# Kernel optimization log

Hardware: AMD Instinct MI355X
Metric: run time of the kernel (lower is better)

## Reference

```python
import jax, jax.numpy as jnp
import numpy as np

EMBED = 768
HEADS = 12
D_K = EMBED // HEADS  # 64


def setup_inputs() -> dict:
    key = jax.random.key(0)
    ks = jax.random.split(key, 9)
    w_scale = EMBED ** -0.5
    inp = {
        "x": jax.random.normal(ks[0], (128, 256, 1, EMBED), dtype=jnp.float32),
        "Wq": jax.random.normal(ks[1], (EMBED, EMBED), dtype=jnp.float32) * w_scale,
        "bq": jax.random.normal(ks[2], (EMBED,), dtype=jnp.float32) * 0.02,
        "Wk": jax.random.normal(ks[3], (EMBED, EMBED), dtype=jnp.float32) * w_scale,
        "bk": jax.random.normal(ks[4], (EMBED,), dtype=jnp.float32) * 0.02,
        "Wv": jax.random.normal(ks[5], (EMBED, EMBED), dtype=jnp.float32) * w_scale,
        "bv": jax.random.normal(ks[6], (EMBED,), dtype=jnp.float32) * 0.02,
        "Wo": jax.random.normal(ks[7], (EMBED, EMBED), dtype=jnp.float32) * w_scale,
        "bo": jax.random.normal(ks[8], (EMBED,), dtype=jnp.float32) * 0.02,
    }
    return inp


def reference(x, Wq, bq, Wk, bk, Wv, bv, Wo, bo):
    # x: (n_rows r, n_cols i/j, batch n, embed)
    R, C, B, E = x.shape
    H, Dk = HEADS, D_K
    # tied-row scaling: d_k^{-1/2} / sqrt(n_rows)
    scaling = (Dk ** -0.5) / np.sqrt(R).astype(np.float32)

    q = (x @ Wq.T + bq).reshape(R, C, B, H, Dk) * scaling
    k = (x @ Wk.T + bk).reshape(R, C, B, H, Dk)
    v = (x @ Wv.T + bv).reshape(R, C, B, H, Dk)

    # scores summed over rows r and head dim d -> (h, n, i, j)
    scores = jnp.einsum('rinhd,rjnhd->hnij', q, k)
    probs = jax.nn.softmax(scores, axis=-1)  # dropout p=0 -> identity

    # shared attention applied per row
    c = jnp.einsum('hnij,rjnhd->rinhd', probs, v).reshape(R, C, B, E)
    out = c @ Wo.T + bo
    return (out, probs)
```

## Files before the change

### kernel.cpp

```cpp
#include <hip/hip_runtime.h>
#include <math.h>

typedef short bf16x8 __attribute__((ext_vector_type(8)));
typedef float f32x4 __attribute__((ext_vector_type(4)));
typedef unsigned short ushort8 __attribute__((ext_vector_type(8)));
typedef unsigned short ushort4v __attribute__((ext_vector_type(4)));

constexpr int R = 128, Cc = 256, E = 768, H = 12;
constexpr int M = R * Cc;
constexpr size_t TOK = (size_t)M * E;

__device__ __forceinline__ unsigned short f2b(float f) {
  unsigned int u = __float_as_uint(f);
  u += 0x7fff + ((u >> 16) & 1);
  return (unsigned short)(u >> 16);
}

__device__ __forceinline__ void ldst16(const unsigned short* g, unsigned short* l) {
  __builtin_amdgcn_global_load_lds(
      (const __attribute__((address_space(1))) unsigned int*)g,
      (__attribute__((address_space(3))) unsigned int*)l, 16, 0, 0);
}

__global__ __launch_bounds__(256) void cvt_bf16(const float* __restrict__ in,
                                                unsigned short* __restrict__ out,
                                                int n8) {
  int i = blockIdx.x * 256 + threadIdx.x;
  if (i >= n8) return;
  const float4* p = (const float4*)in;
  float4 a = p[2 * i], b = p[2 * i + 1];
  ushort8 o;
  o[0] = f2b(a.x); o[1] = f2b(a.y); o[2] = f2b(a.z); o[3] = f2b(a.w);
  o[4] = f2b(b.x); o[5] = f2b(b.y); o[6] = f2b(b.z); o[7] = f2b(b.w);
  ((ushort8*)out)[i] = o;
}

__device__ __forceinline__ void stage64(const unsigned short* __restrict__ A, int lda,
                                        const unsigned short* __restrict__ B, int ldb,
                                        int k0, unsigned short* As, unsigned short* Bs,
                                        int wv, int ln, int srow, int scol) {
#pragma unroll
  for (int t = 0; t < 4; ++t) {
    const int ch = wv * 4 + t;
    const int row = ch * 8 + srow;
    ldst16(A + (size_t)row * lda + k0 + scol, As + ch * 512 + ln * 8);
    ldst16(B + (size_t)row * ldb + k0 + scol, Bs + ch * 512 + ln * 8);
  }
}

__device__ __forceinline__ void gemm128(const unsigned short* __restrict__ A, int lda,
                                        const unsigned short* __restrict__ B, int ldb,
                                        int K, unsigned short* As, unsigned short* Bs,
                                        int wv, int ln, int wm, int wn,
                                        f32x4 (&acc)[4][4]) {
  const int srow = ln >> 3;
  const int scol = ((ln & 7) ^ srow) * 8;
  stage64(A, lda, B, ldb, 0, As, Bs, wv, ln, srow, scol);
  __syncthreads();
  int cur = 0;
  for (int k0 = 0; k0 < K; k0 += 64) {
    if (k0 + 64 < K)
      stage64(A, lda, B, ldb, k0 + 64, As + (cur ^ 1) * 8192, Bs + (cur ^ 1) * 8192,
              wv, ln, srow, scol);
    const unsigned short* Ab = As + cur * 8192;
    const unsigned short* Bb = Bs + cur * 8192;
#pragma unroll
    for (int dk = 0; dk < 2; ++dk) {
      const int rc = ((dk * 4 + (ln >> 4)) ^ (ln & 7)) * 8;
      bf16x8 a[4], b[4];
#pragma unroll
      for (int i = 0; i < 4; ++i)
        a[i] = *(const bf16x8*)(Ab + (wm + i * 16 + (ln & 15)) * 64 + rc);
#pragma unroll
      for (int j = 0; j < 4; ++j)
        b[j] = *(const bf16x8*)(Bb + (wn + j * 16 + (ln & 15)) * 64 + rc);
#pragma unroll
      for (int i = 0; i < 4; ++i)
#pragma unroll
        for (int j = 0; j < 4; ++j)
          acc[i][j] = __builtin_amdgcn_mfma_f32_16x16x32_bf16(a[i], b[j], acc[i][j], 0, 0, 0);
    }
    __syncthreads();
    cur ^= 1;
  }
}

__global__ __launch_bounds__(256) void qkv_proj(
    const unsigned short* __restrict__ A, const unsigned short* __restrict__ B,
    const float* __restrict__ bq, const float* __restrict__ bk,
    const float* __restrict__ bv, unsigned short* __restrict__ q2,
    unsigned short* __restrict__ k2, unsigned short* __restrict__ v3, float scaling) {
  __shared__ unsigned short As[2 * 128 * 64];
  __shared__ unsigned short Bs[2 * 128 * 64];
  const int tid = threadIdx.x, wv = tid >> 6, ln = tid & 63;
  const unsigned p = blockIdx.x + blockIdx.y * 18;
  const unsigned l = (p & 7) * 576 + (p >> 3);
  const int bx = l % 18, by = l / 18;
  const int n0 = bx * 128, m0 = by * 128;
  const int wm = (wv & 1) * 64, wn = (wv >> 1) * 64;
  f32x4 acc[4][4] = {};
  gemm128(A + (size_t)m0 * 768, 768, B + (size_t)n0 * 768, 768, 768,
          As, Bs, wv, ln, wm, wn, acc);

  const int region = bx / 6;
  const float* bias = region == 0 ? bq : (region == 1 ? bk : bv);
  const float sc = region == 0 ? scaling : 1.0f;
  const int nq0 = n0 - region * 768;
#pragma unroll
  for (int j = 0; j < 4; ++j) {
    const int np = nq0 + wn + j * 16 + (ln & 15);
    const int h = np >> 6, d = np & 63;
    const float bn = bias[np];
#pragma unroll
    for (int i = 0; i < 4; ++i) {
      const int mb = m0 + wm + i * 16 + (ln >> 4) * 4;
      if (region < 2) {
        unsigned short* dst = region == 0 ? q2 : k2;
#pragma unroll
        for (int r = 0; r < 4; ++r) {
          const int m = mb + r;
          const int ic = m & 255, rr = m >> 8;
          dst[(size_t)h * 2097152 + (size_t)ic * 8192 + rr * 64 + d] =
              f2b((acc[i][j][r] + bn) * sc);
        }
      } else {
        const int jc = mb & 255, rr = mb >> 8;
        ushort4v o;
#pragma unroll
        for (int r = 0; r < 4; ++r) o[r] = f2b(acc[i][j][r] + bn);
        *(ushort4v*)(v3 + (size_t)h * 2097152 + ((size_t)rr * 64 + d) * 256 + jc) = o;
      }
    }
  }
}

__global__ __launch_bounds__(256) void qk_gemm(const unsigned short* __restrict__ q2,
                                               const unsigned short* __restrict__ k2,
                                               float* __restrict__ Sp) {
  __shared__ unsigned short As[2 * 128 * 64];
  __shared__ unsigned short Bs[2 * 128 * 64];
  const int tid = threadIdx.x, wv = tid >> 6, ln = tid & 63;
  const int i0 = (blockIdx.x & 1) * 128, j0 = (blockIdx.x >> 1) * 128;
  const int h = blockIdx.y, kc = blockIdx.z;
  const int wm = (wv & 1) * 64, wn = (wv >> 1) * 64;
  f32x4 acc[4][4] = {};
  const unsigned short* Ap = q2 + (size_t)h * 2097152 + (size_t)i0 * 8192 + kc * 1024;
  const unsigned short* Bp = k2 + (size_t)h * 2097152 + (size_t)j0 * 8192 + kc * 1024;
  gemm128(Ap, 8192, Bp, 8192, 1024, As, Bs, wv, ln, wm, wn, acc);
  float* out = Sp + ((size_t)kc * H + h) * 65536;
#pragma unroll
  for (int j = 0; j < 4; ++j) {
    const int jj = j0 + wn + j * 16 + (ln & 15);
#pragma unroll
    for (int i = 0; i < 4; ++i)
#pragma unroll
      for (int r = 0; r < 4; ++r) {
        const int ii = i0 + wm + i * 16 + (ln >> 4) * 4 + r;
        out[(size_t)ii * 256 + jj] = acc[i][j][r];
      }
  }
}

__global__ __launch_bounds__(256) void softmax_k(const float* __restrict__ Sp,
                                                 float* __restrict__ P,
                                                 unsigned short* __restrict__ Pb) {
  const int row = blockIdx.x, j = threadIdx.x;
  const size_t stride = (size_t)H * Cc * Cc;
  const size_t base = (size_t)row * Cc + j;
  float s = 0.f;
#pragma unroll
  for (int c = 0; c < 8; ++c) s += Sp[base + c * stride];
  float m = s;
#pragma unroll
  for (int o = 32; o > 0; o >>= 1) m = fmaxf(m, __shfl_xor(m, o));
  __shared__ float sm[4], ss[4];
  const int wid = j >> 6, lane = j & 63;
  if (lane == 0) sm[wid] = m;
  __syncthreads();
  m = fmaxf(fmaxf(sm[0], sm[1]), fmaxf(sm[2], sm[3]));
  float e = expf(s - m);
  float t = e;
#pragma unroll
  for (int o = 32; o > 0; o >>= 1) t += __shfl_xor(t, o);
  if (lane == 0) ss[wid] = t;
  __syncthreads();
  t = ss[0] + ss[1] + ss[2] + ss[3];
  const float p = e / t;
  P[base] = p;
  Pb[base] = f2b(p);
}

__global__ __launch_bounds__(256) void pv_gemm(const unsigned short* __restrict__ P,
                                               const unsigned short* __restrict__ V,
                                               unsigned short* __restrict__ Co) {
  __shared__ unsigned short As[2 * 128 * 64];
  __shared__ unsigned short Bs[2 * 128 * 64];
  const int tid = threadIdx.x, wv = tid >> 6, ln = tid & 63;
  const unsigned p = blockIdx.x + blockIdx.y * 128;
  const unsigned l = (p & 7) * 192 + (p >> 3);
  const int bx = l & 127, h = l >> 7;
  const int i0 = (bx & 1) * 128, n0 = (bx >> 1) * 128;
  const int wm = (wv & 1) * 64, wn = (wv >> 1) * 64;
  f32x4 acc[4][4] = {};
  const unsigned short* Ap = P + (size_t)h * 65536 + (size_t)i0 * 256;
  const unsigned short* Bp = V + (size_t)h * 2097152 + (size_t)n0 * 256;
  gemm128(Ap, 256, Bp, 256, 256, As, Bs, wv, ln, wm, wn, acc);
#pragma unroll
  for (int j = 0; j < 4; ++j) {
    const int n = n0 + wn + j * 16 + (ln & 15);
    const int rr = n >> 6, d = n & 63;
#pragma unroll
    for (int i = 0; i < 4; ++i)
#pragma unroll
      for (int r = 0; r < 4; ++r) {
        const int ii = i0 + wm + i * 16 + (ln >> 4) * 4 + r;
        Co[((size_t)rr * 256 + ii) * 768 + h * 64 + d] = f2b(acc[i][j][r]);
      }
  }
}

__global__ __launch_bounds__(256) void o_proj(const unsigned short* __restrict__ A,
                                              const unsigned short* __restrict__ B,
                                              const float* __restrict__ bias,
                                              float* __restrict__ Y) {
  __shared__ unsigned short As[2 * 128 * 64];
  __shared__ unsigned short Bs[2 * 128 * 64];
  const int tid = threadIdx.x, wv = tid >> 6, ln = tid & 63;
  const unsigned p = blockIdx.x + blockIdx.y * 6;
  const unsigned l = (p & 7) * 192 + (p >> 3);
  const int bx = l % 6, by = l / 6;
  const int n0 = bx * 128, m0 = by * 128;
  const int wm = (wv & 1) * 64, wn = (wv >> 1) * 64;
  f32x4 acc[4][4] = {};
  gemm128(A + (size_t)m0 * 768, 768, B + (size_t)n0 * 768, 768, 768,
          As, Bs, wv, ln, wm, wn, acc);
#pragma unroll
  for (int j = 0; j < 4; ++j) {
    const int n = n0 + wn + j * 16 + (ln & 15);
    const float bn = bias[n];
#pragma unroll
    for (int i = 0; i < 4; ++i)
#pragma unroll
      for (int r = 0; r < 4; ++r) {
        const int m = m0 + wm + i * 16 + (ln >> 4) * 4 + r;
        Y[(size_t)m * 768 + n] = acc[i][j][r] + bn;
      }
  }
}

extern "C" void kernel_launch(void* const* d_in, const int* in_sizes, int n_in,
                              void* d_out, int out_size, void* d_ws, size_t ws_size,
                              hipStream_t stream) {
  const float* x  = (const float*)d_in[0];
  const float* Wq = (const float*)d_in[1];
  const float* bq = (const float*)d_in[2];
  const float* Wk = (const float*)d_in[3];
  const float* bk = (const float*)d_in[4];
  const float* Wv = (const float*)d_in[5];
  const float* bv = (const float*)d_in[6];
  const float* Wo = (const float*)d_in[7];
  const float* bo = (const float*)d_in[8];
  float* out = (float*)d_out;
  float* probs = out + TOK;

  char* ws = (char*)d_ws;
  unsigned short* x_bf  = (unsigned short*)(ws);
  unsigned short* q2    = (unsigned short*)(ws + 50331648);
  unsigned short* k2    = (unsigned short*)(ws + 100663296);
  unsigned short* v3    = (unsigned short*)(ws + 150994944);
  unsigned short* Wq_bf = (unsigned short*)(ws + 201326592);
  unsigned short* Wk_bf = Wq_bf + 589824;
  unsigned short* Wv_bf = Wk_bf + 589824;
  unsigned short* Wo_bf = Wv_bf + 589824;
  float* S_part         = (float*)(ws);
  unsigned short* P_bf  = (unsigned short*)(ws + 25165824);
  unsigned short* c_bf  = q2;

  const float scaling = 0.125f / sqrtf(128.f);

  cvt_bf16<<<12288, 256, 0, stream>>>(x, x_bf, 3145728);
  cvt_bf16<<<288, 256, 0, stream>>>(Wq, Wq_bf, 73728);
  cvt_bf16<<<288, 256, 0, stream>>>(Wk, Wk_bf, 73728);
  cvt_bf16<<<288, 256, 0, stream>>>(Wv, Wv_bf, 73728);
  cvt_bf16<<<288, 256, 0, stream>>>(Wo, Wo_bf, 73728);

  qkv_proj<<<dim3(18, 256), 256, 0, stream>>>(x_bf, Wq_bf, bq, bk, bv,
                                              q2, k2, v3, scaling);

  qk_gemm<<<dim3(4, H, 8), 256, 0, stream>>>(q2, k2, S_part);
  softmax_k<<<H * Cc, 256, 0, stream>>>(S_part, probs, P_bf);
  pv_gemm<<<dim3(128, H), 256, 0, stream>>>(P_bf, v3, c_bf);

  o_proj<<<dim3(6, 256), 256, 0, stream>>>(c_bf, Wo_bf, bo, out);
}
```

Baseline: 537.5 us.

## Restructure GEMM mainloop to keep two tiles of global-to-LDS loads in flight

The shared bf16 GEMM helper now issues the first two K-tiles up front. Each iteration uses a partial vmcnt wait so the next tile's direct-to-LDS loads stay outstanding. It then reads the whole current tile into registers, hits a barrier, and refills that buffer with tile t+2 before running the MFMAs, so global loads overlap the math. In exchange it holds more fragments in registers (a/b for both k-halves) and uses hand-written waitcnt/sched_barrier sequences that depend on the exact count of 8 loads per stage.

After: 492.1 us. -8.5%, faster.

```diff
diff --git a/kernel.cpp b/kernel.cpp
--- a/kernel.cpp
+++ b/kernel.cpp
@@ -55,33 +55,46 @@
                                         f32x4 (&acc)[4][4]) {
   const int srow = ln >> 3;
   const int scol = ((ln & 7) ^ srow) * 8;
+  const int nt = K >> 6;
   stage64(A, lda, B, ldb, 0, As, Bs, wv, ln, srow, scol);
-  __syncthreads();
-  int cur = 0;
-  for (int k0 = 0; k0 < K; k0 += 64) {
-    if (k0 + 64 < K)
-      stage64(A, lda, B, ldb, k0 + 64, As + (cur ^ 1) * 8192, Bs + (cur ^ 1) * 8192,
-              wv, ln, srow, scol);
+  if (nt > 1)
+    stage64(A, lda, B, ldb, 64, As + 8192, Bs + 8192, wv, ln, srow, scol);
+  for (int t = 0; t < nt; ++t) {
+    const int cur = t & 1;
+    if (t + 1 < nt) {
+      asm volatile("s_waitcnt vmcnt(8)" ::: "memory");
+    } else {
+      asm volatile("s_waitcnt vmcnt(0)" ::: "memory");
+    }
+    __builtin_amdgcn_sched_barrier(0);
+    __builtin_amdgcn_s_barrier();
     const unsigned short* Ab = As + cur * 8192;
     const unsigned short* Bb = Bs + cur * 8192;
+    bf16x8 a[2][4], b[2][4];
 #pragma unroll
     for (int dk = 0; dk < 2; ++dk) {
       const int rc = ((dk * 4 + (ln >> 4)) ^ (ln & 7)) * 8;
-      bf16x8 a[4], b[4];
 #pragma unroll
       for (int i = 0; i < 4; ++i)
-        a[i] = *(const bf16x8*)(Ab + (wm + i * 16 + (ln & 15)) * 64 + rc);
+        a[dk][i] = *(const bf16x8*)(Ab + (wm + i * 16 + (ln & 15)) * 64 + rc);
 #pragma unroll
       for (int j = 0; j < 4; ++j)
-        b[j] = *(const bf16x8*)(Bb + (wn + j * 16 + (ln & 15)) * 64 + rc);
+        b[dk][j] = *(const bf16x8*)(Bb + (wn + j * 16 + (ln & 15)) * 64 + rc);
+    }
+    asm volatile("s_waitcnt lgkmcnt(0)" ::: "memory");
+    __builtin_amdgcn_sched_barrier(0);
+    __builtin_amdgcn_s_barrier();
+    if (t + 2 < nt)
+      stage64(A, lda, B, ldb, (t + 2) * 64, As + cur * 8192, Bs + cur * 8192,
+              wv, ln, srow, scol);
+#pragma unroll
+    for (int dk = 0; dk < 2; ++dk)
 #pragma unroll
       for (int i = 0; i < 4; ++i)
 #pragma unroll
         for (int j = 0; j < 4; ++j)
-          acc[i][j] = __builtin_amdgcn_mfma_f32_16x16x32_bf16(a[i], b[j], acc[i][j], 0, 0, 0);
-    }
-    __syncthreads();
-    cur ^= 1;
+          acc[i][j] = __builtin_amdgcn_mfma_f32_16x16x32_bf16(a[dk][i], b[dk][j],
+                                                              acc[i][j], 0, 0, 0);
   }
 }
 
```
